# Performance work log

Hardware: AMD Instinct MI355X
Metric: run time of the kernel (lower is better)

The kernel has to match this reference:

```python
import jax, jax.numpy as jnp
import numpy as np

KERNEL_EPSILON = 0.001


def setup_inputs() -> dict:
    key = jax.random.key(0)
    k1, k2, k3 = jax.random.split(key, 3)
    B, H, S, D = 4, 16, 4096, 64
    return {
        "query": jax.random.normal(k1, (B, H, S, D), dtype=jnp.float32),
        "key": jax.random.normal(k2, (B, H, S, D), dtype=jnp.float32),
        "value": jax.random.normal(k3, (B, H, S, D), dtype=jnp.float32),
        "mask": jnp.ones((B, S), dtype=jnp.float32),
    }


def reference(query, key, value, mask):
    # ReLU feature map + epsilon
    q = jax.nn.relu(query) + KERNEL_EPSILON          # [B,H,S,D]
    k = jax.nn.relu(key) + KERNEL_EPSILON            # [B,H,S,D]
    k = k * mask[:, None, :, None]                   # mask keys
    # kv: [B,H,D,E] = sum_s k[...,s,d] * v[...,s,e]  (done first: linear attention)
    kv = jnp.einsum("bhsd,bhse->bhde", k, value)
    numerator = jnp.einsum("bhsd,bhde->bhse", q, kv)  # [B,H,S,D]
    k_sum = jnp.sum(k, axis=-2)                       # [B,H,D]
    denominator = jnp.einsum("bhsd,bhd->bhs", q, k_sum)[..., None]
    return numerator / denominator
```

## Files before the change

### kernel.cpp

```cpp
#include <hip/hip_runtime.h>


namespace {
constexpr int kB = 4, kH = 16, kS = 4096, kD = 64;
constexpr int kBH = kB * kH;
constexpr float kEps = 0.001f;

constexpr int KVSZ = kD * kD;
constexpr int SEG  = KVSZ + kD;
constexpr int F4PS = SEG / 4;
}

__global__ __launch_bounds__(256, 2)
void pa_kv_partial(const float* __restrict__ key, const float* __restrict__ value,
                   const float* __restrict__ mask, float* __restrict__ P, int ch1) {
  __shared__ float smem[4096];
  __shared__ float ksm[256];

  const int tid  = threadIdx.x;
  const int wid  = tid >> 6;
  const int lane = tid & 63;

  const int bh    = blockIdx.x / ch1;
  const int chunk = blockIdx.x - bh * ch1;
  const int b     = bh >> 4;
  const int rows  = kS / ch1;
  const int s0    = chunk * rows;
  const int tiles = rows >> 5;

  const float* kb = key   + (size_t)bh * kS * kD;
  const float* vb = value + (size_t)bh * kS * kD;
  const float* mb = mask  + (size_t)b * kS;

  float* ksT = smem + wid * 1024;
  float* vsT = smem + wid * 1024 + 512;

  const int lrow = lane >> 4;
  const int lcol = (lane & 15) << 2;
  const int ti   = lane >> 3;
  const int tj   = lane & 7;

  float acc[8][8];
#pragma unroll
  for (int i = 0; i < 8; ++i)
#pragma unroll
    for (int j = 0; j < 8; ++j) acc[i][j] = 0.f;
  float4 ksacc = make_float4(0.f, 0.f, 0.f, 0.f);

  int ts = s0 + wid * 8;
  float4 kq0 = *(const float4*)(kb + (size_t)(ts + lrow) * kD + lcol);
  float4 kq1 = *(const float4*)(kb + (size_t)(ts + 4 + lrow) * kD + lcol);
  float4 vq0 = *(const float4*)(vb + (size_t)(ts + lrow) * kD + lcol);
  float4 vq1 = *(const float4*)(vb + (size_t)(ts + 4 + lrow) * kD + lcol);
  float  m0  = mb[ts + lrow];
  float  m1  = mb[ts + 4 + lrow];

  for (int t = 0; t < tiles; ++t) {
    float4 kt0, kt1;
    kt0.x = (fmaxf(kq0.x, 0.f) + kEps) * m0;
    kt0.y = (fmaxf(kq0.y, 0.f) + kEps) * m0;
    kt0.z = (fmaxf(kq0.z, 0.f) + kEps) * m0;
    kt0.w = (fmaxf(kq0.w, 0.f) + kEps) * m0;
    kt1.x = (fmaxf(kq1.x, 0.f) + kEps) * m1;
    kt1.y = (fmaxf(kq1.y, 0.f) + kEps) * m1;
    kt1.z = (fmaxf(kq1.z, 0.f) + kEps) * m1;
    kt1.w = (fmaxf(kq1.w, 0.f) + kEps) * m1;

    ksacc.x += kt0.x + kt1.x;
    ksacc.y += kt0.y + kt1.y;
    ksacc.z += kt0.z + kt1.z;
    ksacc.w += kt0.w + kt1.w;

    *(float4*)&ksT[lrow * 64 + lcol]       = kt0;
    *(float4*)&ksT[(lrow + 4) * 64 + lcol] = kt1;
    *(float4*)&vsT[lrow * 64 + lcol]       = vq0;
    *(float4*)&vsT[(lrow + 4) * 64 + lcol] = vq1;

    if (t + 1 < tiles) {
      ts += 32;
      kq0 = *(const float4*)(kb + (size_t)(ts + lrow) * kD + lcol);
      kq1 = *(const float4*)(kb + (size_t)(ts + 4 + lrow) * kD + lcol);
      vq0 = *(const float4*)(vb + (size_t)(ts + lrow) * kD + lcol);
      vq1 = *(const float4*)(vb + (size_t)(ts + 4 + lrow) * kD + lcol);
      m0  = mb[ts + lrow];
      m1  = mb[ts + 4 + lrow];
    }

#pragma unroll
    for (int ss = 0; ss < 8; ++ss) {
      const float4 kf0 = *(const float4*)&ksT[ss * 64 + 8 * ti];
      const float4 kf1 = *(const float4*)&ksT[ss * 64 + 8 * ti + 4];
      const float4 vf0 = *(const float4*)&vsT[ss * 64 + 8 * tj];
      const float4 vf1 = *(const float4*)&vsT[ss * 64 + 8 * tj + 4];
      const float ka[8] = {kf0.x, kf0.y, kf0.z, kf0.w, kf1.x, kf1.y, kf1.z, kf1.w};
      const float va[8] = {vf0.x, vf0.y, vf0.z, vf0.w, vf1.x, vf1.y, vf1.z, vf1.w};
#pragma unroll
      for (int i = 0; i < 8; ++i)
#pragma unroll
        for (int j = 0; j < 8; ++j) acc[i][j] = fmaf(ka[i], va[j], acc[i][j]);
    }
  }

  ksacc.x += __shfl_xor(ksacc.x, 16); ksacc.x += __shfl_xor(ksacc.x, 32);
  ksacc.y += __shfl_xor(ksacc.y, 16); ksacc.y += __shfl_xor(ksacc.y, 32);
  ksacc.z += __shfl_xor(ksacc.z, 16); ksacc.z += __shfl_xor(ksacc.z, 32);
  ksacc.w += __shfl_xor(ksacc.w, 16); ksacc.w += __shfl_xor(ksacc.w, 32);
  if (lane < 16) *(float4*)&ksm[wid * 64 + 4 * lane] = ksacc;

#pragma unroll
  for (int w = 0; w < 4; ++w) {
    __syncthreads();
    if (wid == w) {
#pragma unroll
      for (int i = 0; i < 8; ++i)
#pragma unroll
        for (int jj = 0; jj < 2; ++jj) {
          const int j = i * 2 + jj;
          float4 o = make_float4(acc[i][jj * 4 + 0], acc[i][jj * 4 + 1],
                                 acc[i][jj * 4 + 2], acc[i][jj * 4 + 3]);
          float* p = &smem[(size_t)(j * 64 + lane) * 4];
          if (w != 0) {
            const float4 prev = *(const float4*)p;
            o.x += prev.x; o.y += prev.y; o.z += prev.z; o.w += prev.w;
          }
          *(float4*)p = o;
        }
    }
  }
  __syncthreads();

  float* Pd = P + (size_t)blockIdx.x * SEG;
#pragma unroll
  for (int i = 0; i < 4; ++i) {
    const int idx = tid + 256 * i;
    *(float4*)&Pd[(size_t)idx * 4] = *(const float4*)&smem[(size_t)idx * 4];
  }
  if (tid < kD)
    Pd[KVSZ + tid] = ksm[tid] + ksm[64 + tid] + ksm[128 + tid] + ksm[192 + tid];
}

__global__ __launch_bounds__(256)
void pa_reduce(const float* __restrict__ P, float* __restrict__ R, int nseg) {
  const int gid = blockIdx.x * 256 + threadIdx.x;
  if (gid >= kBH * F4PS) return;
  const int bh  = gid / F4PS;
  const int pos = gid - bh * F4PS;

  const float* base = P + (size_t)bh * nseg * SEG + (size_t)pos * 4;
  float ax = 0.f, ay = 0.f, az = 0.f, aw = 0.f;
  for (int c = 0; c < nseg; ++c) {
    const float4 t = *(const float4*)(base + (size_t)c * SEG);
    ax += t.x; ay += t.y; az += t.z; aw += t.w;
  }

  int dpos;
  if (pos < KVSZ / 4) {
    const int j  = pos >> 6, ln = pos & 63;
    const int d  = 8 * (ln >> 3) + (j >> 1);
    const int e4 = 2 * (ln & 7) + (j & 1);
    dpos = d * 16 + e4;
  } else {
    dpos = pos;
  }
  *(float4*)&R[(size_t)bh * SEG + (size_t)dpos * 4] = make_float4(ax, ay, az, aw);
}

__global__ __launch_bounds__(256)
void pa_out(const float* __restrict__ query, const float* __restrict__ R,
            float* __restrict__ out) {
  __shared__ float ost[64 * 68];

  const int tid    = threadIdx.x;
  const int bh     = blockIdx.x >> 4;
  const int rowblk = blockIdx.x & 15;
  const int s      = rowblk * 256 + tid;

  const float* qrow = query + ((size_t)bh * kS + s) * kD;
  const float* Rb   = R + (size_t)bh * SEG;

  float4 acc[16];
#pragma unroll
  for (int e = 0; e < 16; ++e) acc[e] = make_float4(0.f, 0.f, 0.f, 0.f);
  float den = 0.f;

#pragma unroll 4
  for (int d4 = 0; d4 < 16; ++d4) {
    const float4 qv = *(const float4*)(qrow + 4 * d4);
    const float qd[4] = {fmaxf(qv.x, 0.f) + kEps, fmaxf(qv.y, 0.f) + kEps,
                         fmaxf(qv.z, 0.f) + kEps, fmaxf(qv.w, 0.f) + kEps};
#pragma unroll
    for (int dd = 0; dd < 4; ++dd) {
      const int d = 4 * d4 + dd;
      den = fmaf(qd[dd], Rb[KVSZ + d], den);
      const float* kvr = Rb + d * 64;
#pragma unroll
      for (int e = 0; e < 16; ++e) {
        acc[e].x = fmaf(qd[dd], kvr[4 * e + 0], acc[e].x);
        acc[e].y = fmaf(qd[dd], kvr[4 * e + 1], acc[e].y);
        acc[e].z = fmaf(qd[dd], kvr[4 * e + 2], acc[e].z);
        acc[e].w = fmaf(qd[dd], kvr[4 * e + 3], acc[e].w);
      }
    }
  }

  const float inv = 1.0f / den;
#pragma unroll
  for (int e = 0; e < 16; ++e) {
    acc[e].x *= inv; acc[e].y *= inv; acc[e].z *= inv; acc[e].w *= inv;
  }

  float* ob = out + ((size_t)bh * kS + (size_t)rowblk * 256) * kD;
  const int wid = tid >> 6, l = tid & 63;
  for (int bb = 0; bb < 4; ++bb) {
    if (wid == bb) {
#pragma unroll
      for (int e = 0; e < 16; ++e) *(float4*)&ost[l * 68 + 4 * e] = acc[e];
    }
    __syncthreads();
#pragma unroll
    for (int jj = 0; jj < 4; ++jj) {
      const int g = tid + 256 * jj;
      const int r = g >> 4, c = g & 15;
      *(float4*)&ob[(size_t)(bb * 64 + r) * kD + 4 * c] =
          *(const float4*)&ost[r * 68 + 4 * c];
    }
    __syncthreads();
  }
}

extern "C" void kernel_launch(void* const* d_in, const int* in_sizes, int n_in,
                              void* d_out, int out_size, void* d_ws, size_t ws_size,
                              hipStream_t stream) {
  const float* query = (const float*)d_in[0];
  const float* key   = (const float*)d_in[1];
  const float* value = (const float*)d_in[2];
  const float* mask  = (const float*)d_in[3];
  float* outp = (float*)d_out;

  auto need = [](int ch1) -> size_t {
    return (size_t)(kBH * ch1 + kBH) * SEG * sizeof(float);
  };
  int CH1 = 8;
  if (ws_size >= need(16)) CH1 = 16;

  float* P = (float*)d_ws;
  float* R = P + (size_t)kBH * CH1 * SEG;

  hipLaunchKernelGGL(pa_kv_partial, dim3(kBH * CH1), dim3(256), 0, stream,
                     key, value, mask, P, CH1);
  hipLaunchKernelGGL(pa_reduce, dim3((kBH * F4PS + 255) / 256), dim3(256), 0, stream,
                     P, R, CH1);
  hipLaunchKernelGGL(pa_out, dim3(kBH * 16), dim3(256), 0, stream,
                     query, R, outp);
}
```

Baseline: 249.7 us.

## Pipeline value loads into LDS with async global_load_lds triple buffering

Value tiles in the KV-partial kernel are now copied straight from global memory into LDS through async global_load_lds into a three-slot rotating buffer. Key loads are issued two tiles ahead, and the mask is staged once into shared memory. The goal is to hide global memory latency behind the FMA work without staging value data through registers. The cost is more LDS per block, which may reduce occupancy, and hand-written vmcnt waits whose counts must match the number of outstanding loads exactly.

```diff
diff --git a/kernel.cpp b/kernel.cpp
--- a/kernel.cpp
+++ b/kernel.cpp
@@ -11,10 +11,18 @@
 constexpr int F4PS = SEG / 4;
 }
 
+__device__ __forceinline__ void async_cp16(const float* g, float* l) {
+  __builtin_amdgcn_global_load_lds(
+      (const __attribute__((address_space(1))) void*)g,
+      (__attribute__((address_space(3))) void*)l, 16, 0, 0);
+}
+
 __global__ __launch_bounds__(256, 2)
 void pa_kv_partial(const float* __restrict__ key, const float* __restrict__ value,
                    const float* __restrict__ mask, float* __restrict__ P, int ch1) {
-  __shared__ float smem[4096];
+  __shared__ float smemV[3 * 2048];
+  __shared__ float smemK[4 * 512];
+  __shared__ float msk[512];
   __shared__ float ksm[256];
 
   const int tid  = threadIdx.x;
@@ -28,12 +36,17 @@
   const int s0    = chunk * rows;
   const int tiles = rows >> 5;
 
-  const float* kb = key   + (size_t)bh * kS * kD;
-  const float* vb = value + (size_t)bh * kS * kD;
+  const float* kg = key   + (size_t)bh * kS * kD;
+  const float* vg = value + (size_t)bh * kS * kD;
   const float* mb = mask  + (size_t)b * kS;
 
-  float* ksT = smem + wid * 1024;
-  float* vsT = smem + wid * 1024 + 512;
+  for (int i = tid; i < rows; i += 256) msk[i] = mb[s0 + i];
+  __syncthreads();
+
+  float* ksT = smemK + wid * 512;
+  float* v0b = smemV + wid * 512;
+  float* v1b = smemV + 2048 + wid * 512;
+  float* v2b = smemV + 4096 + wid * 512;
 
   const int lrow = lane >> 4;
   const int lcol = (lane & 15) << 2;
@@ -47,59 +60,76 @@
     for (int j = 0; j < 8; ++j) acc[i][j] = 0.f;
   float4 ksacc = make_float4(0.f, 0.f, 0.f, 0.f);
 
-  int ts = s0 + wid * 8;
-  float4 kq0 = *(const float4*)(kb + (size_t)(ts + lrow) * kD + lcol);
-  float4 kq1 = *(const float4*)(kb + (size_t)(ts + 4 + lrow) * kD + lcol);
-  float4 vq0 = *(const float4*)(vb + (size_t)(ts + lrow) * kD + lcol);
-  float4 vq1 = *(const float4*)(vb + (size_t)(ts + 4 + lrow) * kD + lcol);
-  float  m0  = mb[ts + lrow];
-  float  m1  = mb[ts + 4 + lrow];
-
-  for (int t = 0; t < tiles; ++t) {
-    float4 kt0, kt1;
-    kt0.x = (fmaxf(kq0.x, 0.f) + kEps) * m0;
-    kt0.y = (fmaxf(kq0.y, 0.f) + kEps) * m0;
-    kt0.z = (fmaxf(kq0.z, 0.f) + kEps) * m0;
-    kt0.w = (fmaxf(kq0.w, 0.f) + kEps) * m0;
-    kt1.x = (fmaxf(kq1.x, 0.f) + kEps) * m1;
-    kt1.y = (fmaxf(kq1.y, 0.f) + kEps) * m1;
-    kt1.z = (fmaxf(kq1.z, 0.f) + kEps) * m1;
-    kt1.w = (fmaxf(kq1.w, 0.f) + kEps) * m1;
-
-    ksacc.x += kt0.x + kt1.x;
-    ksacc.y += kt0.y + kt1.y;
-    ksacc.z += kt0.z + kt1.z;
-    ksacc.w += kt0.w + kt1.w;
-
-    *(float4*)&ksT[lrow * 64 + lcol]       = kt0;
-    *(float4*)&ksT[(lrow + 4) * 64 + lcol] = kt1;
-    *(float4*)&vsT[lrow * 64 + lcol]       = vq0;
-    *(float4*)&vsT[(lrow + 4) * 64 + lcol] = vq1;
-
-    if (t + 1 < tiles) {
-      ts += 32;
-      kq0 = *(const float4*)(kb + (size_t)(ts + lrow) * kD + lcol);
-      kq1 = *(const float4*)(kb + (size_t)(ts + 4 + lrow) * kD + lcol);
-      vq0 = *(const float4*)(vb + (size_t)(ts + lrow) * kD + lcol);
-      vq1 = *(const float4*)(vb + (size_t)(ts + 4 + lrow) * kD + lcol);
-      m0  = mb[ts + lrow];
-      m1  = mb[ts + 4 + lrow];
-    }
-
-#pragma unroll
-    for (int ss = 0; ss < 8; ++ss) {
-      const float4 kf0 = *(const float4*)&ksT[ss * 64 + 8 * ti];
-      const float4 kf1 = *(const float4*)&ksT[ss * 64 + 8 * ti + 4];
-      const float4 vf0 = *(const float4*)&vsT[ss * 64 + 8 * tj];
-      const float4 vf1 = *(const float4*)&vsT[ss * 64 + 8 * tj + 4];
-      const float ka[8] = {kf0.x, kf0.y, kf0.z, kf0.w, kf1.x, kf1.y, kf1.z, kf1.w};
-      const float va[8] = {vf0.x, vf0.y, vf0.z, vf0.w, vf1.x, vf1.y, vf1.z, vf1.w};
-#pragma unroll
-      for (int i = 0; i < 8; ++i)
-#pragma unroll
-        for (int j = 0; j < 8; ++j) acc[i][j] = fmaf(ka[i], va[j], acc[i][j]);
-    }
-  }
+  const int r0 = wid * 8;
+  float4 kqA0, kqA1, kqB0, kqB1;
+  float mA0, mA1, mB0, mB1;
+
+  async_cp16(vg + (size_t)(s0 + r0 + lrow) * kD + lcol, v0b);
+  async_cp16(vg + (size_t)(s0 + r0 + 4 + lrow) * kD + lcol, v0b + 256);
+  kqA0 = *(const float4*)(kg + (size_t)(s0 + r0 + lrow) * kD + lcol);
+  kqA1 = *(const float4*)(kg + (size_t)(s0 + r0 + 4 + lrow) * kD + lcol);
+  asm volatile("" ::: "memory");
+  async_cp16(vg + (size_t)(s0 + r0 + 32 + lrow) * kD + lcol, v1b);
+  async_cp16(vg + (size_t)(s0 + r0 + 36 + lrow) * kD + lcol, v1b + 256);
+  kqB0 = *(const float4*)(kg + (size_t)(s0 + r0 + 32 + lrow) * kD + lcol);
+  kqB1 = *(const float4*)(kg + (size_t)(s0 + r0 + 36 + lrow) * kD + lcol);
+  asm volatile("" ::: "memory");
+  mA0 = msk[r0 + lrow];      mA1 = msk[r0 + 4 + lrow];
+  mB0 = msk[r0 + 32 + lrow]; mB1 = msk[r0 + 36 + lrow];
+
+  int ts2 = s0 + r0 + 64;
+  int to2 = r0 + 64;
+
+#define PA_RND(KQ0, KQ1, M0, M1, WAITN, ISSUE)                                \
+  {                                                                           \
+    float4 kt0, kt1;                                                          \
+    kt0.x = (fmaxf(KQ0.x, 0.f) + kEps) * M0;                                  \
+    kt0.y = (fmaxf(KQ0.y, 0.f) + kEps) * M0;                                  \
+    kt0.z = (fmaxf(KQ0.z, 0.f) + kEps) * M0;                                  \
+    kt0.w = (fmaxf(KQ0.w, 0.f) + kEps) * M0;                                  \
+    kt1.x = (fmaxf(KQ1.x, 0.f) + kEps) * M1;                                  \
+    kt1.y = (fmaxf(KQ1.y, 0.f) + kEps) * M1;                                  \
+    kt1.z = (fmaxf(KQ1.z, 0.f) + kEps) * M1;                                  \
+    kt1.w = (fmaxf(KQ1.w, 0.f) + kEps) * M1;                                  \
+    ksacc.x += kt0.x + kt1.x; ksacc.y += kt0.y + kt1.y;                       \
+    ksacc.z += kt0.z + kt1.z; ksacc.w += kt0.w + kt1.w;                       \
+    *(float4*)&ksT[lrow * 64 + lcol]       = kt0;                             \
+    *(float4*)&ksT[(lrow + 4) * 64 + lcol] = kt1;                             \
+    if (ISSUE) {                                                              \
+      async_cp16(vg + (size_t)(ts2 + lrow) * kD + lcol, v2b);                 \
+      async_cp16(vg + (size_t)(ts2 + 4 + lrow) * kD + lcol, v2b + 256);       \
+      KQ0 = *(const float4*)(kg + (size_t)(ts2 + lrow) * kD + lcol);          \
+      KQ1 = *(const float4*)(kg + (size_t)(ts2 + 4 + lrow) * kD + lcol);      \
+      M0 = msk[to2 + lrow];  M1 = msk[to2 + 4 + lrow];                        \
+      ts2 += 32; to2 += 32;                                                   \
+    }                                                                         \
+    asm volatile("s_waitcnt vmcnt(" #WAITN ")" ::: "memory");                 \
+    _Pragma("unroll")                                                         \
+    for (int ss = 0; ss < 8; ++ss) {                                          \
+      const float4 kf0 = *(const float4*)&ksT[ss * 64 + 8 * ti];              \
+      const float4 kf1 = *(const float4*)&ksT[ss * 64 + 8 * ti + 4];          \
+      const float4 vf0 = *(const float4*)&v0b[ss * 64 + 8 * tj];              \
+      const float4 vf1 = *(const float4*)&v0b[ss * 64 + 8 * tj + 4];          \
+      const float ka[8] = {kf0.x, kf0.y, kf0.z, kf0.w,                        \
+                           kf1.x, kf1.y, kf1.z, kf1.w};                       \
+      const float va_[8] = {vf0.x, vf0.y, vf0.z, vf0.w,                       \
+                            vf1.x, vf1.y, vf1.z, vf1.w};                      \
+      _Pragma("unroll")                                                       \
+      for (int i = 0; i < 8; ++i)                                             \
+        _Pragma("unroll")                                                     \
+        for (int j = 0; j < 8; ++j)                                           \
+          acc[i][j] = fmaf(ka[i], va_[j], acc[i][j]);                         \
+    }                                                                         \
+    { float* rot_ = v0b; v0b = v1b; v1b = v2b; v2b = rot_; }                  \
+  }
+
+  for (int t = 0; t < tiles - 2; t += 2) {
+    PA_RND(kqA0, kqA1, mA0, mA1, 8, true)
+    PA_RND(kqB0, kqB1, mB0, mB1, 8, true)
+  }
+  PA_RND(kqA0, kqA1, mA0, mA1, 4, false)
+  PA_RND(kqB0, kqB1, mB0, mB1, 0, false)
+#undef PA_RND
 
   ksacc.x += __shfl_xor(ksacc.x, 16); ksacc.x += __shfl_xor(ksacc.x, 32);
   ksacc.y += __shfl_xor(ksacc.y, 16); ksacc.y += __shfl_xor(ksacc.y, 32);
@@ -118,7 +148,7 @@
           const int j = i * 2 + jj;
           float4 o = make_float4(acc[i][jj * 4 + 0], acc[i][jj * 4 + 1],
                                  acc[i][jj * 4 + 2], acc[i][jj * 4 + 3]);
-          float* p = &smem[(size_t)(j * 64 + lane) * 4];
+          float* p = &smemV[(size_t)(j * 64 + lane) * 4];
           if (w != 0) {
             const float4 prev = *(const float4*)p;
             o.x += prev.x; o.y += prev.y; o.z += prev.z; o.w += prev.w;
@@ -133,7 +163,7 @@
 #pragma unroll
   for (int i = 0; i < 4; ++i) {
     const int idx = tid + 256 * i;
-    *(float4*)&Pd[(size_t)idx * 4] = *(const float4*)&smem[(size_t)idx * 4];
+    *(float4*)&Pd[(size_t)idx * 4] = *(const float4*)&smemV[(size_t)idx * 4];
   }
   if (tid < kD)
     Pd[KVSZ + tid] = ksm[tid] + ksm[64 + tid] + ksm[128 + tid] + ksm[192 + tid];
```

Result: slower. 282.0 us (+12.9%).
